# Kernel optimization log

Measured on AMD Instinct MI355X. Metric: run time of the kernel, lower is better.

## Reference

```python
import jax, jax.numpy as jnp
import numpy as np

TEMP = 100000.0  # extreme temperature -> softmax ~ hard argmax of nearest past keyframe


def setup_inputs() -> dict:
    key = jax.random.key(0)
    k1, k2, k3 = jax.random.split(key, 3)
    B, T_in, N, T_out = 16, 64, 52, 4096
    root_positions = jax.random.normal(k1, (B, T_in, 3), dtype=jnp.float32)
    joint_rotations_ortho6d = jax.random.normal(k2, (B, T_in, N, 6), dtype=jnp.float32)
    input_frame_indices = jnp.sort(jax.random.randint(k3, (T_in,), 0, T_out, dtype=jnp.int64))
    # guarantee a past keyframe exists for every target (avoids all -inf column / NaN)
    input_frame_indices = input_frame_indices.at[0].set(0)
    target_frame_indices = jnp.arange(T_out, dtype=jnp.int64)
    return {
        "root_positions": root_positions,
        "joint_rotations_ortho6d": joint_rotations_ortho6d,
        "input_frame_indices": input_frame_indices,
        "target_frame_indices": target_frame_indices,
    }


def _zero_velocity(root_positions, joint_rotations_ortho6d,
                   input_frame_indices, target_frame_indices, nb_joints):
    # [T_in, T_out] timestamp differences; future keyframes (diff > 0) masked out
    diff = (input_frame_indices[:, None] - target_frame_indices[None, :]).astype(jnp.float32)
    diff = jnp.where(diff > 0.0, -jnp.inf, diff)
    diff = diff - jnp.max(diff, axis=0, keepdims=True)
    weights = jax.nn.softmax(TEMP * diff, axis=0)  # [T_in, T_out], ~one-hot per column

    # root position: [B, T_in, 3] x [T_in, T_out] -> [B, T_out, 3]
    root = jnp.einsum('btc,ts->bsc', root_positions, weights)
    B, T_out = root.shape[0], root.shape[1]
    # repeat across joints -> [B, T_out, N, 3]
    joint_positions = jnp.broadcast_to(root[:, :, None, :], (B, T_out, nb_joints, 3))
    joint_positions = jnp.asarray(joint_positions)

    # rotations: [B, T_in, N, 6] x [T_in, T_out] -> [B, T_out, N, 6]
    joint_rotations = jnp.einsum('btnc,ts->bsnc', joint_rotations_ortho6d, weights)
    return joint_positions, joint_rotations


def _pad_time(x, t_in):
    # prepend first frame repeated (t_in - 1) times, append last frame once
    front = jnp.repeat(x[:, :1], t_in - 1, axis=1)
    return jnp.concatenate([front, x, x[:, -1:]], axis=1)


def reference(root_positions, joint_rotations_ortho6d,
              input_frame_indices, target_frame_indices):
    nb_joints = joint_rotations_ortho6d.shape[2]
    jp, jr = _zero_velocity(root_positions, joint_rotations_ortho6d,
                            input_frame_indices, target_frame_indices, nb_joints)
    t_in = input_frame_indices.shape[0]
    return _pad_time(jp, t_in), _pad_time(jr, t_in)
```

## Files before the change

kernel.cpp:

```cpp
#include <hip/hip_runtime.h>

constexpr int B     = 16;
constexpr int T_IN  = 64;
constexpr int NJ    = 52;
constexpr int T_OUT = 4096;
constexpr int T_PAD = T_OUT + T_IN;

constexpr int JP_ROW4 = NJ * 3 / 4;
constexpr int JR_ROW4 = NJ * 6 / 4;
constexpr int NROWS   = B * T_PAD;
constexpr int NP4     = NROWS * JP_ROW4;
constexpr int NR4     = NROWS * JR_ROW4;
constexpr int TOTAL4  = NP4 + NR4;

typedef float f4 __attribute__((ext_vector_type(4)));

__global__ __launch_bounds__(256) void zv_fused(
    const float* __restrict__ root,
    const float* __restrict__ rot,
    const int*   __restrict__ idx,
    f4*          __restrict__ out4)
{
    __shared__ int sidx[T_IN];
    if (threadIdx.x < T_IN) sidx[threadIdx.x] = idx[threadIdx.x];
    __syncthreads();

    const int i = blockIdx.x * 256 + threadIdx.x;
    if (i >= TOTAL4) return;

    const bool is_jp = (i < NP4);
    int row, w;
    if (is_jp) {
        row = i / JP_ROW4;  w = i - row * JP_ROW4;
    } else {
        const int j = i - NP4;
        row = j / JR_ROW4;  w = j - row * JR_ROW4;
    }
    const int b     = row / T_PAD;
    const int s_out = row - b * T_PAD;
    int s = s_out - (T_IN - 1);
    s = s < 0 ? 0 : (s > T_OUT - 1 ? T_OUT - 1 : s);

    int ub = 0;
    #pragma unroll
    for (int step = 64; step > 0; step >>= 1)
        if (ub + step <= T_IN && sidx[ub + step - 1] <= s) ub += step;
    const int m = sidx[ub - 1];
    int lo = 0;
    #pragma unroll
    for (int step = 32; step > 0; step >>= 1)
        if (sidx[lo + step - 1] < m) lo += step;
    const int   k   = ub - lo;
    const float inv = 1.0f / (float)k;

    if (is_jp) {
        const float* rp = root + (size_t)(b * T_IN + lo) * 3;
        float r0 = rp[0], r1 = rp[1], r2 = rp[2];
        for (int t = 1; t < k; ++t) { r0 += rp[3*t]; r1 += rp[3*t+1]; r2 += rp[3*t+2]; }
        r0 *= inv; r1 *= inv; r2 *= inv;
        const int md = w % 3;
        const float x0 = md == 0 ? r0 : (md == 1 ? r1 : r2);
        const float x1 = md == 0 ? r1 : (md == 1 ? r2 : r0);
        const float x2 = md == 0 ? r2 : (md == 1 ? r0 : r1);
        f4 v; v.x = x0; v.y = x1; v.z = x2; v.w = x0;
        __builtin_nontemporal_store(v, &out4[i]);
    } else {
        const f4* src = (const f4*)rot + ((size_t)(b * T_IN + lo) * JR_ROW4 + w);
        f4 acc = src[0];
        if (k > 1) {
            for (int t = 1; t < k; ++t) acc += src[(size_t)t * JR_ROW4];
            acc *= inv;
        }
        __builtin_nontemporal_store(acc, &out4[i]);
    }
}

extern "C" void kernel_launch(void* const* d_in, const int* in_sizes, int n_in,
                              void* d_out, int out_size, void* d_ws, size_t ws_size,
                              hipStream_t stream) {
    const float* root = (const float*)d_in[0];
    const float* rot  = (const float*)d_in[1];
    const int*   idx  = (const int*)d_in[2];
    f4* out4 = (f4*)d_out;

    const int grid = (TOTAL4 + 255) / 256;
    hipLaunchKernelGGL(zv_fused, dim3(grid), dim3(256), 0, stream,
                       root, rot, idx, out4);
}
```

Measured before the change: 27.98 us.

## Map one block per output time step and share keyframe search

The kernel now launches one block per padded output time step rather than one thread per output float4. Each block runs the keyframe binary search once, computes the root means for all batches into shared memory, then loops over all batch/joint columns for that time step. This removes the per-thread index search and division work. The cost is that each block's writes are strided across batch rows instead of one contiguous range. The nontemporal stores also become plain stores, and there are fewer, larger blocks (4160).

```diff
diff --git a/kernel.cpp b/kernel.cpp
--- a/kernel.cpp
+++ b/kernel.cpp
@@ -10,34 +10,25 @@
 constexpr int JR_ROW4 = NJ * 6 / 4;
 constexpr int NROWS   = B * T_PAD;
 constexpr int NP4     = NROWS * JP_ROW4;
-constexpr int NR4     = NROWS * JR_ROW4;
-constexpr int TOTAL4  = NP4 + NR4;
+
+constexpr int JP_COL4 = B * JP_ROW4;
+constexpr int JR_COL4 = B * JR_ROW4;
 
 typedef float f4 __attribute__((ext_vector_type(4)));
 
-__global__ __launch_bounds__(256) void zv_fused(
+__global__ __launch_bounds__(256) void zv_col(
     const float* __restrict__ root,
     const float* __restrict__ rot,
     const int*   __restrict__ idx,
     f4*          __restrict__ out4)
 {
     __shared__ int sidx[T_IN];
-    if (threadIdx.x < T_IN) sidx[threadIdx.x] = idx[threadIdx.x];
+    __shared__ f4  srm[B];
+    const int tid = threadIdx.x;
+    if (tid < T_IN) sidx[tid] = idx[tid];
     __syncthreads();
 
-    const int i = blockIdx.x * 256 + threadIdx.x;
-    if (i >= TOTAL4) return;
-
-    const bool is_jp = (i < NP4);
-    int row, w;
-    if (is_jp) {
-        row = i / JP_ROW4;  w = i - row * JP_ROW4;
-    } else {
-        const int j = i - NP4;
-        row = j / JR_ROW4;  w = j - row * JR_ROW4;
-    }
-    const int b     = row / T_PAD;
-    const int s_out = row - b * T_PAD;
+    const int s_out = blockIdx.x;
     int s = s_out - (T_IN - 1);
     s = s < 0 ? 0 : (s > T_OUT - 1 ? T_OUT - 1 : s);
 
@@ -53,25 +44,38 @@
     const int   k   = ub - lo;
     const float inv = 1.0f / (float)k;
 
-    if (is_jp) {
-        const float* rp = root + (size_t)(b * T_IN + lo) * 3;
+    if (tid < B) {
+        const float* rp = root + (size_t)(tid * T_IN + lo) * 3;
         float r0 = rp[0], r1 = rp[1], r2 = rp[2];
-        for (int t = 1; t < k; ++t) { r0 += rp[3*t]; r1 += rp[3*t+1]; r2 += rp[3*t+2]; }
-        r0 *= inv; r1 *= inv; r2 *= inv;
+        for (int q = 1; q < k; ++q) { r0 += rp[3*q]; r1 += rp[3*q+1]; r2 += rp[3*q+2]; }
+        f4 v; v.x = r0 * inv; v.y = r1 * inv; v.z = r2 * inv; v.w = 0.f;
+        srm[tid] = v;
+    }
+    __syncthreads();
+
+    for (int f = tid; f < JP_COL4; f += 256) {
+        const int b = f / JP_ROW4;
+        const int w = f - b * JP_ROW4;
+        const f4 rm = srm[b];
         const int md = w % 3;
+        const float r0 = rm.x, r1 = rm.y, r2 = rm.z;
         const float x0 = md == 0 ? r0 : (md == 1 ? r1 : r2);
         const float x1 = md == 0 ? r1 : (md == 1 ? r2 : r0);
         const float x2 = md == 0 ? r2 : (md == 1 ? r0 : r1);
         f4 v; v.x = x0; v.y = x1; v.z = x2; v.w = x0;
-        __builtin_nontemporal_store(v, &out4[i]);
-    } else {
+        out4[(size_t)(b * T_PAD + s_out) * JP_ROW4 + w] = v;
+    }
+
+    for (int f = tid; f < JR_COL4; f += 256) {
+        const int b = f / JR_ROW4;
+        const int w = f - b * JR_ROW4;
         const f4* src = (const f4*)rot + ((size_t)(b * T_IN + lo) * JR_ROW4 + w);
-        f4 acc = src[0];
+        f4 a = src[0];
         if (k > 1) {
-            for (int t = 1; t < k; ++t) acc += src[(size_t)t * JR_ROW4];
-            acc *= inv;
+            for (int q = 1; q < k; ++q) a += src[(size_t)q * JR_ROW4];
+            a *= inv;
         }
-        __builtin_nontemporal_store(acc, &out4[i]);
+        out4[NP4 + (size_t)(b * T_PAD + s_out) * JR_ROW4 + w] = a;
     }
 }
 
@@ -83,7 +87,6 @@
     const int*   idx  = (const int*)d_in[2];
     f4* out4 = (f4*)d_out;
 
-    const int grid = (TOTAL4 + 255) / 256;
-    hipLaunchKernelGGL(zv_fused, dim3(grid), dim3(256), 0, stream,
+    hipLaunchKernelGGL(zv_col, dim3(T_PAD), dim3(256), 0, stream,
                        root, rot, idx, out4);
 }
```

New measurement: 28.25 us. About the same (+1.0%).
